# Optimization experiments

Measured on AMD Instinct MI355X. Metric: run time of the kernel, lower is better.

The kernel has to match this reference:

```python
import jax, jax.numpy as jnp
import numpy as np

N_NODES = 100000


def gcn_conv(x, src, dst, W, b, n):
    # PyG GCNConv: add self-loops, symmetric deg^-1/2 normalization,
    # linear transform, gather->scatter-add aggregation, + bias.
    loop = jnp.arange(n, dtype=src.dtype)
    s = jnp.concatenate([src, loop])
    d = jnp.concatenate([dst, loop])
    deg = jax.ops.segment_sum(jnp.ones_like(d, dtype=x.dtype), d, num_segments=n)
    dinv = jnp.where(deg > 0, jax.lax.rsqrt(deg), jnp.zeros_like(deg))
    norm = dinv[s] * dinv[d]            # [E+N]
    h = x @ W                            # [N, out] (transform before propagate)
    msg = h[s] * norm[:, None]           # gather + scale
    out = jax.ops.segment_sum(msg, d, num_segments=n)  # scatter-add to dst
    return out + b


def setup_inputs() -> dict:
    key = jax.random.key(0)
    k = jax.random.split(key, 6)
    n, e, c_in, hid, c_out = N_NODES, 2500000, 5, 32, 1
    x = jax.random.normal(k[0], (n, c_in), dtype=jnp.float32)
    edge_index = jax.random.randint(k[1], (2, e), 0, n, dtype=jnp.int64)
    # Glorot-style init for GCN weights, zero bias (PyG default)
    W1 = jax.random.normal(k[2], (c_in, hid), dtype=jnp.float32) * (1.0 / np.sqrt(c_in))
    b1 = jnp.zeros((hid,), dtype=jnp.float32)
    W2 = jax.random.normal(k[3], (hid, c_out), dtype=jnp.float32) * (1.0 / np.sqrt(hid))
    b2 = jnp.zeros((c_out,), dtype=jnp.float32)
    return {"x": x, "edge_index": edge_index, "W1": W1, "b1": b1, "W2": W2, "b2": b2}


def reference(x, edge_index, W1, b1, W2, b2):
    n = x.shape[0]
    src, dst = edge_index[0], edge_index[1]
    h = jax.nn.relu(gcn_conv(x, src, dst, W1, b1, n))
    # dropout p=0.3 is identity at inference (training=False)
    return jax.nn.sigmoid(gcn_conv(h, src, dst, W2, b2, n))
```

## Files before the change

kernel.cpp:

```cpp
#include <hip/hip_runtime.h>
#include <math.h>


#define NB_SHIFT  8
#define BNODES    256
#define NBMAX     512
#define CAP       8192
#define CAP_SHIFT 13
#define CHUNK     8192
#define PBLK      256

__global__ void k_init(int* __restrict__ bcur) {
    int b = threadIdx.x;
    if (b < NBMAX) bcur[b] = b << CAP_SHIFT;
}

__global__ __launch_bounds__(PBLK) void k_part(const int* __restrict__ src,
                                               const int* __restrict__ dst, int E,
                                               int* __restrict__ bcur,
                                               int* __restrict__ pairs) {
    __shared__ int sp[CHUNK];
    __shared__ unsigned short sb[CHUNK];
    __shared__ int cnt[NBMAX], ofs[NBMAX], cur[NBMAX], gbase[NBMAX];
    __shared__ int tsum[PBLK];
    int tid = threadIdx.x;
    int base = blockIdx.x * CHUNK;
    int m = min(CHUNK, E - base);

    for (int b = tid; b < NBMAX; b += PBLK) cnt[b] = 0;
    __syncthreads();
    for (int i = tid; i < m; i += PBLK)
        atomicAdd(&cnt[dst[base + i] >> NB_SHIFT], 1);
    __syncthreads();
    int b0 = tid * 2;
    int s0 = cnt[b0], s1 = cnt[b0 + 1], tot = s0 + s1;
    tsum[tid] = tot;
    __syncthreads();
    for (int off = 1; off < PBLK; off <<= 1) {
        int u = (tid >= off) ? tsum[tid - off] : 0;
        __syncthreads();
        tsum[tid] += u;
        __syncthreads();
    }
    int pre = tsum[tid] - tot;
    ofs[b0] = pre;      ofs[b0 + 1] = pre + s0;
    cur[b0] = pre;      cur[b0 + 1] = pre + s0;
    __syncthreads();
    for (int i = tid; i < m; i += PBLK) {
        int s = src[base + i], d = dst[base + i];
        int b = d >> NB_SHIFT;
        int p = atomicAdd(&cur[b], 1);
        sp[p] = ((d & (BNODES - 1)) << 24) | s;
        sb[p] = (unsigned short)b;
    }
    __syncthreads();
    for (int b = tid; b < NBMAX; b += PBLK) {
        int c = cnt[b];
        gbase[b] = c ? atomicAdd(&bcur[b], c) : 0;
    }
    __syncthreads();
    for (int i = tid; i < m; i += PBLK) {
        int b = sb[i];
        pairs[gbase[b] + (i - ofs[b])] = sp[i];
    }
}

__global__ __launch_bounds__(BNODES) void k_sortb(int* __restrict__ pairs,
                                                  const int* __restrict__ bcur,
                                                  const float* __restrict__ x,
                                                  float* __restrict__ dinv,
                                                  float* __restrict__ xs,
                                                  int* __restrict__ nofs,
                                                  int* __restrict__ deg, int n) {
    __shared__ int stage[CAP];
    __shared__ int stage2[CAP];
    __shared__ int cnt[BNODES], cur[BNODES];
    int tid = threadIdx.x;
    int b = blockIdx.x;
    int base = b << CAP_SHIFT;
    int len = min(bcur[b] - base, CAP);

    for (int i = tid; i < len; i += BNODES) stage[i] = pairs[base + i];
    cnt[tid] = 0;
    __syncthreads();
    for (int i = tid; i < len; i += BNODES)
        atomicAdd(&cnt[((unsigned)stage[i]) >> 24], 1);
    __syncthreads();
    int v = cnt[tid];
    for (int off = 1; off < BNODES; off <<= 1) {
        int u = (tid >= off) ? cnt[tid - off] : 0;
        __syncthreads();
        cnt[tid] += u;
        __syncthreads();
    }
    int pos = cnt[tid] - v;
    cur[tid] = pos;
    int node = (b << NB_SHIFT) + tid;
    if (node < n) {
        nofs[node] = base + pos;
        deg[node] = v;
        float di = rsqrtf((float)v + 1.0f);
        dinv[node] = di;
        const float* xr = x + (size_t)node * 5;
        float* xo = xs + ((size_t)node << 3);
#pragma unroll
        for (int k = 0; k < 5; ++k) xo[k] = xr[k] * di;
    }
    __syncthreads();
    for (int i = tid; i < len; i += BNODES) {
        int vv = stage[i];
        int p = atomicAdd(&cur[((unsigned)vv) >> 24], 1);
        stage2[p] = vv & 0x00FFFFFF;
    }
    __syncthreads();
    for (int i = tid; i < len; i += BNODES) pairs[base + i] = stage2[i];
}

__global__ __launch_bounds__(256) void k_agg1(const int* __restrict__ pairs,
                                              const int* __restrict__ nofs,
                                              const int* __restrict__ deg,
                                              const float* __restrict__ xs,
                                              const float* __restrict__ dinv,
                                              const float* __restrict__ W1,
                                              const float* __restrict__ b1,
                                              const float* __restrict__ W2,
                                              float* __restrict__ h2s, int n) {
    __shared__ float w1[160], bb1[32], w2[32];
    int tid = threadIdx.x;
    if (tid < 160) w1[tid] = W1[tid];
    else if (tid < 192) bb1[tid - 160] = b1[tid - 160];
    else if (tid < 224) w2[tid - 192] = W2[tid - 192];
    __syncthreads();
    int node = blockIdx.x * 128 + (tid >> 1);
    int half = tid & 1;
    if (node >= n) return;
    int beg = nofs[node], dg = deg[node];
    float a0 = 0.f, a1 = 0.f, a2 = 0.f, a3 = 0.f, a4 = 0.f;
    if (!half) {
        const float* xo = xs + ((size_t)node << 3);
        a0 = xo[0]; a1 = xo[1]; a2 = xo[2]; a3 = xo[3]; a4 = xo[4];
    }
    for (int e = beg + half; e < beg + dg; e += 2) {
        int s = pairs[e];
        const float* xr = xs + ((size_t)s << 3);
        float4 q = *(const float4*)xr;
        float q4 = xr[4];
        a0 += q.x; a1 += q.y; a2 += q.z; a3 += q.w; a4 += q4;
    }
    a0 += __shfl_xor(a0, 1); a1 += __shfl_xor(a1, 1); a2 += __shfl_xor(a2, 1);
    a3 += __shfl_xor(a3, 1); a4 += __shfl_xor(a4, 1);
    if (half) return;
    float di = dinv[node];
    a0 *= di; a1 *= di; a2 *= di; a3 *= di; a4 *= di;
    float sum = 0.f;
#pragma unroll
    for (int c = 0; c < 32; ++c) {
        float z = bb1[c] + a0 * w1[c] + a1 * w1[32 + c] + a2 * w1[64 + c]
                         + a3 * w1[96 + c] + a4 * w1[128 + c];
        sum += fmaxf(z, 0.f) * w2[c];
    }
    h2s[node] = sum * di;
}

__global__ __launch_bounds__(256) void k_agg2(const int* __restrict__ pairs,
                                              const int* __restrict__ nofs,
                                              const int* __restrict__ deg,
                                              const float* __restrict__ h2s,
                                              const float* __restrict__ dinv,
                                              const float* __restrict__ b2,
                                              float* __restrict__ out, int n) {
    int tid = threadIdx.x;
    int node = blockIdx.x * 128 + (tid >> 1);
    int half = tid & 1;
    if (node >= n) return;
    int beg = nofs[node], dg = deg[node];
    float a = 0.f;
    for (int e = beg + half; e < beg + dg; e += 2) a += h2s[pairs[e]];
    a += __shfl_xor(a, 1);
    if (half) return;
    float v = dinv[node] * (a + h2s[node]) + b2[0];
    out[node] = 1.0f / (1.0f + __expf(-v));
}

extern "C" void kernel_launch(void* const* d_in, const int* in_sizes, int n_in,
                              void* d_out, int out_size, void* d_ws, size_t ws_size,
                              hipStream_t stream) {
    const float* x  = (const float*)d_in[0];
    const int*   ei = (const int*)d_in[1];
    const float* W1 = (const float*)d_in[2];
    const float* b1 = (const float*)d_in[3];
    const float* W2 = (const float*)d_in[4];
    const float* b2 = (const float*)d_in[5];
    float* out = (float*)d_out;

    const int n = in_sizes[0] / 5;
    const int E = in_sizes[1] / 2;
    const int* src = ei;
    const int* dst = ei + E;
    const int nb = (n + BNODES - 1) >> NB_SHIFT;

    int* wsi = (int*)d_ws;
    int*   pairs = wsi;
    int*   nofs  = wsi + ((size_t)(nb + 1) << CAP_SHIFT);
    int*   deg   = nofs + n;
    float* dinv  = (float*)(deg + n);
    float* h2s   = dinv + n;
    float* xs    = h2s + n;
    int*   bcur  = (int*)(xs + (size_t)8 * n);

    const int nchunk = (E + CHUNK - 1) / CHUNK;
    const int nagg   = (n + 127) / 128;

    k_init<<<1, NBMAX, 0, stream>>>(bcur);
    k_part<<<nchunk, PBLK, 0, stream>>>(src, dst, E, bcur, pairs);
    k_sortb<<<nb, BNODES, 0, stream>>>(pairs, bcur, x, dinv, xs, nofs, deg, n);
    k_agg1<<<nagg, 256, 0, stream>>>(pairs, nofs, deg, xs, dinv, W1, b1, W2, h2s, n);
    k_agg2<<<nagg, 256, 0, stream>>>(pairs, nofs, deg, h2s, dinv, b2, out, n);
}
```

Baseline: 162.8 us.

## Replace shared-memory atomics with ballot-based warp match in partition and bucket sort

Both counting-sort stages now build per-wavefront histograms and compute scatter ranks using ballot-based key matching (9 or 8 ballots per element) instead of LDS atomicAdd. This removes atomic contention and gives a deterministic ordering within each wavefront. The bucket sort also drops its staging copy and re-reads pairs from global memory for its two passes. The cost is many extra ballot and popcount instructions per element, plus a larger per-wave histogram.

```diff
diff --git a/kernel.cpp b/kernel.cpp
--- a/kernel.cpp
+++ b/kernel.cpp
@@ -4,15 +4,27 @@
 
 #define NB_SHIFT  8
 #define BNODES    256
-#define NBMAX     512
+#define NBK       512
 #define CAP       8192
 #define CAP_SHIFT 13
 #define CHUNK     8192
 #define PBLK      256
+#define NW        4
+
+template <int BITS>
+__device__ __forceinline__ unsigned long long grp_mask(int k, bool valid) {
+    unsigned long long m = __ballot(valid ? 1 : 0);
+#pragma unroll
+    for (int i = 0; i < BITS; ++i) {
+        unsigned long long b = __ballot((k >> i) & 1);
+        m &= ((k >> i) & 1) ? b : ~b;
+    }
+    return m;
+}
 
 __global__ void k_init(int* __restrict__ bcur) {
     int b = threadIdx.x;
-    if (b < NBMAX) bcur[b] = b << CAP_SHIFT;
+    if (b < NBK) bcur[b] = b << CAP_SHIFT;
 }
 
 __global__ __launch_bounds__(PBLK) void k_part(const int* __restrict__ src,
@@ -21,19 +33,37 @@
                                                int* __restrict__ pairs) {
     __shared__ int sp[CHUNK];
     __shared__ unsigned short sb[CHUNK];
-    __shared__ int cnt[NBMAX], ofs[NBMAX], cur[NBMAX], gbase[NBMAX];
+    __shared__ int hw[NW * NBK];
+    __shared__ int ofs[NBK];
+    __shared__ int gbase[NBK];
     __shared__ int tsum[PBLK];
-    int tid = threadIdx.x;
+    int tid = threadIdx.x, lane = tid & 63, w = tid >> 6;
     int base = blockIdx.x * CHUNK;
     int m = min(CHUNK, E - base);
-
-    for (int b = tid; b < NBMAX; b += PBLK) cnt[b] = 0;
-    __syncthreads();
-    for (int i = tid; i < m; i += PBLK)
-        atomicAdd(&cnt[dst[base + i] >> NB_SHIFT], 1);
-    __syncthreads();
+    int iters = (m + PBLK - 1) / PBLK;
+
+    for (int i = tid; i < NW * NBK; i += PBLK) hw[i] = 0;
+    __syncthreads();
+    int* hwr = hw + w * NBK;
+
+    for (int it = 0; it < iters; ++it) {
+        int i = it * PBLK + tid;
+        bool valid = i < m;
+        int k = valid ? (dst[base + i] >> NB_SHIFT) : 0;
+        unsigned long long g = grp_mask<9>(k, valid);
+        if (valid && lane == (__ffsll((long long)g) - 1))
+            hwr[k] += __popcll(g);
+    }
+    __syncthreads();
+
     int b0 = tid * 2;
-    int s0 = cnt[b0], s1 = cnt[b0 + 1], tot = s0 + s1;
+    int h0[NW], h1[NW], s0 = 0, s1 = 0;
+#pragma unroll
+    for (int j = 0; j < NW; ++j) {
+        h0[j] = hw[j * NBK + b0];     s0 += h0[j];
+        h1[j] = hw[j * NBK + b0 + 1]; s1 += h1[j];
+    }
+    int tot = s0 + s1;
     tsum[tid] = tot;
     __syncthreads();
     for (int off = 1; off < PBLK; off <<= 1) {
@@ -43,22 +73,36 @@
         __syncthreads();
     }
     int pre = tsum[tid] - tot;
-    ofs[b0] = pre;      ofs[b0 + 1] = pre + s0;
-    cur[b0] = pre;      cur[b0 + 1] = pre + s0;
-    __syncthreads();
-    for (int i = tid; i < m; i += PBLK) {
-        int s = src[base + i], d = dst[base + i];
-        int b = d >> NB_SHIFT;
-        int p = atomicAdd(&cur[b], 1);
-        sp[p] = ((d & (BNODES - 1)) << 24) | s;
-        sb[p] = (unsigned short)b;
-    }
-    __syncthreads();
-    for (int b = tid; b < NBMAX; b += PBLK) {
-        int c = cnt[b];
-        gbase[b] = c ? atomicAdd(&bcur[b], c) : 0;
-    }
-    __syncthreads();
+    ofs[b0] = pre;  ofs[b0 + 1] = pre + s0;
+    int r0 = pre, r1 = pre + s0;
+#pragma unroll
+    for (int j = 0; j < NW; ++j) {
+        hw[j * NBK + b0] = r0;     r0 += h0[j];
+        hw[j * NBK + b0 + 1] = r1; r1 += h1[j];
+    }
+    gbase[b0]     = s0 ? atomicAdd(&bcur[b0], s0) : 0;
+    gbase[b0 + 1] = s1 ? atomicAdd(&bcur[b0 + 1], s1) : 0;
+    __syncthreads();
+
+    for (int it = 0; it < iters; ++it) {
+        int i = it * PBLK + tid;
+        bool valid = i < m;
+        int s = 0, d = 0;
+        if (valid) { s = src[base + i]; d = dst[base + i]; }
+        int k = valid ? (d >> NB_SHIFT) : 0;
+        unsigned long long g = grp_mask<9>(k, valid);
+        int rank = __popcll(g & ((1ull << lane) - 1ull));
+        int pb = valid ? hwr[k] : 0;
+        if (valid) {
+            int p = pb + rank;
+            sp[p] = ((d & (BNODES - 1)) << 24) | s;
+            sb[p] = (unsigned short)k;
+        }
+        if (valid && lane == (__ffsll((long long)g) - 1))
+            hwr[k] = pb + __popcll(g);
+    }
+    __syncthreads();
+
     for (int i = tid; i < m; i += PBLK) {
         int b = sb[i];
         pairs[gbase[b] + (i - ofs[b])] = sp[i];
@@ -72,34 +116,49 @@
                                                   float* __restrict__ xs,
                                                   int* __restrict__ nofs,
                                                   int* __restrict__ deg, int n) {
-    __shared__ int stage[CAP];
     __shared__ int stage2[CAP];
-    __shared__ int cnt[BNODES], cur[BNODES];
-    int tid = threadIdx.x;
+    __shared__ int hw[NW * BNODES];
+    __shared__ int scn[BNODES];
+    int tid = threadIdx.x, lane = tid & 63, w = tid >> 6;
     int b = blockIdx.x;
     int base = b << CAP_SHIFT;
     int len = min(bcur[b] - base, CAP);
-
-    for (int i = tid; i < len; i += BNODES) stage[i] = pairs[base + i];
-    cnt[tid] = 0;
-    __syncthreads();
-    for (int i = tid; i < len; i += BNODES)
-        atomicAdd(&cnt[((unsigned)stage[i]) >> 24], 1);
-    __syncthreads();
-    int v = cnt[tid];
+    int iters = (len + BNODES - 1) / BNODES;
+
+    for (int i = tid; i < NW * BNODES; i += BNODES) hw[i] = 0;
+    __syncthreads();
+    int* hwr = hw + w * BNODES;
+
+    for (int it = 0; it < iters; ++it) {
+        int i = it * BNODES + tid;
+        bool valid = i < len;
+        int k = valid ? (int)(((unsigned)pairs[base + i]) >> 24) : 0;
+        unsigned long long g = grp_mask<8>(k, valid);
+        if (valid && lane == (__ffsll((long long)g) - 1))
+            hwr[k] += __popcll(g);
+    }
+    __syncthreads();
+
+    int hv[NW], tot = 0;
+#pragma unroll
+    for (int j = 0; j < NW; ++j) { hv[j] = hw[j * BNODES + tid]; tot += hv[j]; }
+    scn[tid] = tot;
+    __syncthreads();
     for (int off = 1; off < BNODES; off <<= 1) {
-        int u = (tid >= off) ? cnt[tid - off] : 0;
-        __syncthreads();
-        cnt[tid] += u;
-        __syncthreads();
-    }
-    int pos = cnt[tid] - v;
-    cur[tid] = pos;
+        int u = (tid >= off) ? scn[tid - off] : 0;
+        __syncthreads();
+        scn[tid] += u;
+        __syncthreads();
+    }
+    int pos = scn[tid] - tot;
+    int r = pos;
+#pragma unroll
+    for (int j = 0; j < NW; ++j) { hw[j * BNODES + tid] = r; r += hv[j]; }
     int node = (b << NB_SHIFT) + tid;
     if (node < n) {
         nofs[node] = base + pos;
-        deg[node] = v;
-        float di = rsqrtf((float)v + 1.0f);
+        deg[node] = tot;
+        float di = rsqrtf((float)tot + 1.0f);
         dinv[node] = di;
         const float* xr = x + (size_t)node * 5;
         float* xo = xs + ((size_t)node << 3);
@@ -107,10 +166,18 @@
         for (int k = 0; k < 5; ++k) xo[k] = xr[k] * di;
     }
     __syncthreads();
-    for (int i = tid; i < len; i += BNODES) {
-        int vv = stage[i];
-        int p = atomicAdd(&cur[((unsigned)vv) >> 24], 1);
-        stage2[p] = vv & 0x00FFFFFF;
+
+    for (int it = 0; it < iters; ++it) {
+        int i = it * BNODES + tid;
+        bool valid = i < len;
+        int v = valid ? pairs[base + i] : 0;
+        int k = (int)(((unsigned)v) >> 24);
+        unsigned long long g = grp_mask<8>(k, valid);
+        int rank = __popcll(g & ((1ull << lane) - 1ull));
+        int pb = valid ? hwr[k] : 0;
+        if (valid) stage2[pb + rank] = v & 0x00FFFFFF;
+        if (valid && lane == (__ffsll((long long)g) - 1))
+            hwr[k] = pb + __popcll(g);
     }
     __syncthreads();
     for (int i = tid; i < len; i += BNODES) pairs[base + i] = stage2[i];
@@ -211,7 +278,7 @@
     const int nchunk = (E + CHUNK - 1) / CHUNK;
     const int nagg   = (n + 127) / 128;
 
-    k_init<<<1, NBMAX, 0, stream>>>(bcur);
+    k_init<<<1, NBK, 0, stream>>>(bcur);
     k_part<<<nchunk, PBLK, 0, stream>>>(src, dst, E, bcur, pairs);
     k_sortb<<<nb, BNODES, 0, stream>>>(pairs, bcur, x, dinv, xs, nofs, deg, n);
     k_agg1<<<nagg, 256, 0, stream>>>(pairs, nofs, deg, xs, dinv, W1, b1, W2, h2s, n);
```

Measured after the change: 207.1 us. 27.2% more time.
